# Optimization experiments

Measured on AMD Instinct MI355X. Metric: run time of the kernel, lower is better.

## Reference

```python
import jax, jax.numpy as jnp
import numpy as np

D_MODEL = 512
N_HEADS = 8
D_K = D_MODEL // N_HEADS


def setup_inputs() -> dict:
    key = jax.random.key(0)
    ks = jax.random.split(key, 7)
    s = 1.0 / np.sqrt(D_MODEL)
    return {
        "x": jax.random.normal(ks[0], (2, 4096, D_MODEL), dtype=jnp.float32),
        "W_q": jax.random.normal(ks[1], (D_MODEL, D_MODEL), dtype=jnp.float32) * s,
        "W_k": jax.random.normal(ks[2], (D_MODEL, D_MODEL), dtype=jnp.float32) * s,
        "W_v": jax.random.normal(ks[3], (D_MODEL, D_MODEL), dtype=jnp.float32) * s,
        "b_v": jax.random.normal(ks[4], (D_MODEL,), dtype=jnp.float32) * s,
        "W_o": jax.random.normal(ks[5], (D_MODEL, D_MODEL), dtype=jnp.float32) * s,
        "b_o": jax.random.normal(ks[6], (D_MODEL,), dtype=jnp.float32) * s,
    }


def _split_heads(t):
    # [N, S, d_model] -> [N, H, S, d_k]
    N, S, _ = t.shape
    return t.reshape(N, S, N_HEADS, D_K).transpose(0, 2, 1, 3)


def reference(x, W_q, W_k, W_v, b_v, W_o, b_o):
    N, S, _ = x.shape
    # nn.Linear computes x @ W.T (+ b)
    Q = _split_heads(x @ W_q.T)
    K = _split_heads(x @ W_k.T)
    V = _split_heads(x @ W_v.T + b_v)
    scale = jnp.sqrt(jnp.asarray(D_K, x.dtype))
    scores = jnp.einsum('nhqd,nhkd->nhqk', Q, K) / scale  # [N,H,S,S]
    causal = jnp.tril(jnp.ones((S, S), dtype=bool))
    scores = jnp.where(causal, scores, -jnp.inf)
    attn = jax.nn.softmax(scores, axis=-1)
    out = jnp.einsum('nhqk,nhkd->nhqd', attn, V)  # [N,H,S,d_k]
    out = out.transpose(0, 2, 1, 3).reshape(N, S, D_MODEL)
    return out @ W_o.T + b_o
```

## Files before the change

### kernel.cpp

```cpp
#include <hip/hip_runtime.h>
#include <hip/hip_bf16.h>

#define NB 2
#define SEQ 4096
#define DM 512
#define NH 8
#define DKH 64
#define MTOT (NB*SEQ)

typedef __attribute__((ext_vector_type(4))) float f32x4;
typedef __attribute__((ext_vector_type(16))) float f32x16;
typedef __attribute__((ext_vector_type(8))) short bf16x8;
typedef __attribute__((ext_vector_type(2))) unsigned uint2v;

__device__ inline unsigned short f2bf(float f) {
    union { float f; unsigned int u; } v; v.f = f;
    unsigned int r = v.u + 0x7FFFu + ((v.u >> 16) & 1u);
    return (unsigned short)(r >> 16);
}
__device__ inline float bf2f(unsigned short u) {
    union { unsigned int v; float f; } x; x.v = ((unsigned int)u) << 16; return x.f;
}

#define QSCALE 0.18033688011112042f

__global__ void cast_kernel(const float* __restrict__ x, const float* __restrict__ wq,
                            const float* __restrict__ wk, const float* __restrict__ wv,
                            const float* __restrict__ wo, unsigned short* __restrict__ dst) {
    const int NX = MTOT*DM;
    const int NW = DM*DM;
    int i4 = blockIdx.x * blockDim.x + threadIdx.x;
    long e = (long)i4 * 4;
    if (e >= NX + 4L*NW) return;
    const float* src; long off;
    if (e < NX)           { src = x;  off = e; }
    else if (e < NX+NW)   { src = wq; off = e - NX; }
    else if (e < NX+2*NW) { src = wk; off = e - NX - NW; }
    else if (e < NX+3*NW) { src = wv; off = e - NX - 2*NW; }
    else                  { src = wo; off = e - NX - 3*NW; }
    float4 v = *reinterpret_cast<const float4*>(src + off);
    ushort4 o;
    o.x = f2bf(v.x); o.y = f2bf(v.y); o.z = f2bf(v.z); o.w = f2bf(v.w);
    *reinterpret_cast<ushort4*>(dst + e) = o;
}

template<int MODE>
__global__ __launch_bounds__(256, 2) void gemm_bt(
    const unsigned short* __restrict__ A,
    const unsigned short* __restrict__ B,
    const float* __restrict__ bias,
    unsigned short* __restrict__ Qh, unsigned short* __restrict__ Kh,
    unsigned short* __restrict__ Vt,
    float* __restrict__ Cout)
{
    const int K = 512;
    __shared__ __align__(16) unsigned short As[128*64];
    __shared__ __align__(16) unsigned short Bs[128*64];
    int tid = threadIdx.x;
    int wid = tid >> 6, lane = tid & 63;
    int wr = wid >> 1, wc = wid & 1;
    int brow = blockIdx.x * 128;
    int bcol = blockIdx.y * 128;
    int l15 = lane & 15, l4 = lane >> 4;

    f32x4 acc[4][4] = {};

    for (int kt = 0; kt < K/64; ++kt) {
        __syncthreads();
        #pragma unroll
        for (int i = 0; i < 4; ++i) {
            int rbase = i*32 + wid*8;
            int row = rbase + (lane >> 3);
            int csrc = (lane & 7) ^ (row & 7);
            const unsigned short* asrc = A + (long)(brow+row)*K + kt*64 + csrc*8;
            __builtin_amdgcn_global_load_lds(
                (const __attribute__((address_space(1))) unsigned int*)asrc,
                (__attribute__((address_space(3))) unsigned int*)&As[rbase*64], 16, 0, 0);
            const unsigned short* bsrc = B + (long)(bcol+row)*K + kt*64 + csrc*8;
            __builtin_amdgcn_global_load_lds(
                (const __attribute__((address_space(1))) unsigned int*)bsrc,
                (__attribute__((address_space(3))) unsigned int*)&Bs[rbase*64], 16, 0, 0);
        }
        __syncthreads();
        #pragma unroll
        for (int kk = 0; kk < 2; ++kk) {
            bf16x8 af[4], bfr[4];
            #pragma unroll
            for (int mi = 0; mi < 4; ++mi) {
                int row = wr*64 + mi*16 + l15;
                int colb = (kk*32 + l4*8) * 2;
                af[mi] = *reinterpret_cast<const bf16x8*>(
                    reinterpret_cast<const char*>(As) + row*128 + (colb ^ ((row&7)<<4)));
            }
            #pragma unroll
            for (int ni = 0; ni < 4; ++ni) {
                int row = wc*64 + ni*16 + l15;
                int colb = (kk*32 + l4*8) * 2;
                bfr[ni] = *reinterpret_cast<const bf16x8*>(
                    reinterpret_cast<const char*>(Bs) + row*128 + (colb ^ ((row&7)<<4)));
            }
            #pragma unroll
            for (int mi = 0; mi < 4; ++mi)
                #pragma unroll
                for (int ni = 0; ni < 4; ++ni)
                    acc[mi][ni] = __builtin_amdgcn_mfma_f32_16x16x32_bf16(af[mi], bfr[ni], acc[mi][ni], 0, 0, 0);
        }
    }

    #pragma unroll
    for (int mi = 0; mi < 4; ++mi) {
        #pragma unroll
        for (int ni = 0; ni < 4; ++ni) {
            #pragma unroll
            for (int r = 0; r < 4; ++r) {
                int row = brow + wr*64 + mi*16 + l4*4 + r;
                int col = bcol + wc*64 + ni*16 + l15;
                float v = acc[mi][ni][r];
                if (MODE == 0) {
                    int which = col >> 9;
                    int cw = col & 511;
                    int h = cw >> 6, d = cw & 63;
                    int b = row >> 12, s = row & 4095;
                    int bh = b*NH + h;
                    if (which == 0) {
                        Qh[((long)(bh*SEQ + s))*DKH + d] = f2bf(v * QSCALE);
                    } else if (which == 1) {
                        Kh[((long)(bh*SEQ + s))*DKH + d] = f2bf(v);
                    } else {
                        Vt[((long)(bh*DKH + d))*SEQ + s] = f2bf(v + bias[cw]);
                    }
                } else {
                    Cout[(long)row*DM + col] = v + bias[col];
                }
            }
        }
    }
}

#define PV_STEP_M(SV, VLS, KS, B0, OD0, OD1)  do {                                 \
        unsigned c0, c1, c2, c3;                                                   \
        float t0 = SV[B0+0], t1 = SV[B0+1], t2 = SV[B0+2], t3 = SV[B0+3];          \
        float t4 = SV[B0+4], t5 = SV[B0+5], t6 = SV[B0+6], t7 = SV[B0+7];          \
        asm("v_cvt_pk_bf16_f32 %0, %1, %2" : "=v"(c0) : "v"(t0), "v"(t1));         \
        asm("v_cvt_pk_bf16_f32 %0, %1, %2" : "=v"(c1) : "v"(t2), "v"(t3));         \
        asm("v_cvt_pk_bf16_f32 %0, %1, %2" : "=v"(c2) : "v"(t4), "v"(t5));         \
        asm("v_cvt_pk_bf16_f32 %0, %1, %2" : "=v"(c3) : "v"(t6), "v"(t7));         \
        uint2v sw0 = __builtin_amdgcn_permlane32_swap(c0, c2, false, false);       \
        uint2v sw1 = __builtin_amdgcn_permlane32_swap(c1, c3, false, false);       \
        union { unsigned u[4]; bf16x8 v; } pu;                                     \
        pu.u[0] = sw0[0]; pu.u[1] = sw1[0]; pu.u[2] = sw0[1]; pu.u[3] = sw1[1];    \
        bf16x8 vf0 = *reinterpret_cast<const bf16x8*>(VLS + l31*128      + (((KS)*32 + hi*16) ^ swz)); \
        OD0 = __builtin_amdgcn_mfma_f32_32x32x16_bf16(vf0, pu.v, OD0, 0, 0, 0);    \
        bf16x8 vf1 = *reinterpret_cast<const bf16x8*>(VLS + (32+l31)*128 + (((KS)*32 + hi*16) ^ swz)); \
        OD1 = __builtin_amdgcn_mfma_f32_32x32x16_bf16(vf1, pu.v, OD1, 0, 0, 0);    \
    } while (0)

__global__ __launch_bounds__(256, 4) void attn_split(
    const unsigned short* __restrict__ Qh,
    const unsigned short* __restrict__ Kh,
    const unsigned short* __restrict__ Vt,
    unsigned short* __restrict__ pO0, unsigned short* __restrict__ pO1,
    float* __restrict__ pml)
{
    __shared__ __align__(16) unsigned short Kc[2][64*64];
    __shared__ __align__(16) unsigned short Vc[2][64*64];
    const int tid = threadIdx.x;
    const int wid = tid >> 6, lane = tid & 63;
    const int g = wid & 1, p = wid >> 1;
    const int l31 = lane & 31;
    const int hi  = lane >> 5;

    const int id   = blockIdx.x;
    const int xcd  = id & 7;
    const int rest = id >> 3;
    const int bh   = xcd + ((rest & 1) << 3);
    const int rem  = rest >> 1;
    const int t    = 63 - (rem >> 1);
    const int c    = rem & 1;

    const unsigned short* Qbase = Qh + (long)bh*SEQ*DKH;
    const unsigned short* Kbase = Kh + (long)bh*SEQ*DKH;
    const unsigned short* Vbase = Vt + (long)bh*DKH*SEQ;

    const int q0w = t*64 + g*32;
    const int q   = q0w + l31;
    const int nu  = (t >= c) ? (((t - c) >> 1) + 1) : 0;
    const int swz = (l31 & 7) << 4;

    bf16x8 qf[4];
    #pragma unroll
    for (int kk = 0; kk < 4; ++kk)
        qf[kk] = *reinterpret_cast<const bf16x8*>(Qbase + (long)q*DKH + kk*16 + hi*8);

    auto STAGE = [&](int b, int key0) {
        #pragma unroll
        for (int ii = 0; ii < 2; ++ii) {
            const int rbase = wid*16 + ii*8;
            const int row = rbase + (lane >> 3);
            const int ck = (lane & 7) ^ (row & 7);
            const unsigned short* ksrc = Kbase + (long)(key0 + row)*DKH + ck*8;
            __builtin_amdgcn_global_load_lds(
                (const __attribute__((address_space(1))) unsigned int*)ksrc,
                (__attribute__((address_space(3))) unsigned int*)&Kc[b][rbase*64], 16, 0, 0);
            const unsigned short* vsrc = Vbase + (long)row*SEQ + key0 + ck*8;
            __builtin_amdgcn_global_load_lds(
                (const __attribute__((address_space(1))) unsigned int*)vsrc,
                (__attribute__((address_space(3))) unsigned int*)&Vc[b][rbase*64], 16, 0, 0);
        }
    };

    float m = -1e30f, lsum = 0.f;
    f32x16 od0 = {}, od1 = {};

    if (nu > 0) STAGE(0, c << 6);
    __syncthreads();
    int cur = 0;

    #pragma unroll 1
    for (int s = 0; s < nu; ++s) {
        const int u = c + 2*s;
        if (s + 1 < nu) STAGE(cur ^ 1, (u + 2) << 6);
        const char* kl = reinterpret_cast<const char*>(&Kc[cur][0]) + p*32*128;
        const char* vl = reinterpret_cast<const char*>(&Vc[cur][0]);

        bf16x8 kfr[4];
        #pragma unroll
        for (int kk = 0; kk < 4; ++kk)
            kfr[kk] = *reinterpret_cast<const bf16x8*>(kl + l31*128 + ((kk*32 + hi*16) ^ swz));
        f32x16 sv = {};
        __builtin_amdgcn_s_setprio(1);
        #pragma unroll
        for (int kk = 0; kk < 4; ++kk)
            sv = __builtin_amdgcn_mfma_f32_32x32x16_bf16(kfr[kk], qf[kk], sv, 0, 0, 0);
        __builtin_amdgcn_s_setprio(0);

        if (u == t) {
            const int kbase = (u << 6) + (p << 5);
            #pragma unroll
            for (int r = 0; r < 16; ++r) {
                const int ko = (r&3) + 8*(r>>2) + 4*hi;
                if (kbase + ko > q) sv[r] = -1e30f;
            }
        }

        float m0 = fmaxf(sv[0],  fmaxf(sv[1],  sv[2]));
        float m1 = fmaxf(sv[3],  fmaxf(sv[4],  sv[5]));
        float m2 = fmaxf(sv[6],  fmaxf(sv[7],  sv[8]));
        float m3 = fmaxf(sv[9],  fmaxf(sv[10], sv[11]));
        float m4 = fmaxf(sv[12], fmaxf(sv[13], sv[14]));
        float pmax = fmaxf(fmaxf(m0, fmaxf(m1, m2)), fmaxf(sv[15], fmaxf(m3, m4)));
        {
            uint2v pr = __builtin_amdgcn_permlane32_swap(__float_as_uint(pmax), __float_as_uint(pmax), false, false);
            pmax = fmaxf(__uint_as_float(pr[0]), __uint_as_float(pr[1]));
        }
        if (__any(pmax > m + 6.0f)) {
            const float mn = fmaxf(m, pmax);
            const float alpha = __builtin_amdgcn_exp2f(m - mn);
            m = mn;
            lsum *= alpha;
            #pragma unroll
            for (int r = 0; r < 16; ++r) { od0[r] *= alpha; od1[r] *= alpha; }
        }

        float rs = 0.f;
        #pragma unroll
        for (int r = 0; r < 16; ++r) {
            sv[r] = __builtin_amdgcn_exp2f(sv[r] - m);
            rs += sv[r];
        }
        lsum += rs;

        __builtin_amdgcn_s_setprio(1);
        PV_STEP_M(sv, vl, (2*p),     0, od0, od1);
        PV_STEP_M(sv, vl, (2*p + 1), 8, od0, od1);
        __builtin_amdgcn_s_setprio(0);

        __syncthreads();
        cur ^= 1;
    }

    char*  sod = reinterpret_cast<char*>(&Kc[g][0]);
    float* sml = reinterpret_cast<float*>(&Vc[g][0]);
    const int lswz = (lane & 7) << 4;
    if (p == 1) {
        #pragma unroll
        for (int i = 0; i < 4; ++i) {
            *reinterpret_cast<f32x4*>(sod + lane*128 + ((i*16) ^ lswz)) =
                (f32x4){od0[i*4+0], od0[i*4+1], od0[i*4+2], od0[i*4+3]};
            *reinterpret_cast<f32x4*>(sod + lane*128 + (((i+4)*16) ^ lswz)) =
                (f32x4){od1[i*4+0], od1[i*4+1], od1[i*4+2], od1[i*4+3]};
        }
        sml[lane*2]     = m;
        sml[lane*2 + 1] = lsum;
    }
    __syncthreads();
    if (p == 0) {
        const float pm  = sml[lane*2];
        const float plv = sml[lane*2 + 1];
        const float mn = fmaxf(m, pm);
        const float a0 = __builtin_amdgcn_exp2f(m - mn);
        const float a1 = __builtin_amdgcn_exp2f(pm - mn);
        m = mn;
        lsum = lsum*a0 + plv*a1;
        #pragma unroll
        for (int i = 0; i < 4; ++i) {
            f32x4 t0 = *reinterpret_cast<const f32x4*>(sod + lane*128 + ((i*16) ^ lswz));
            f32x4 t1 = *reinterpret_cast<const f32x4*>(sod + lane*128 + (((i+4)*16) ^ lswz));
            #pragma unroll
            for (int k = 0; k < 4; ++k) {
                od0[i*4+k] = od0[i*4+k]*a0 + t0[k]*a1;
                od1[i*4+k] = od1[i*4+k]*a0 + t1[k]*a1;
            }
        }
        {
            uint2v pr = __builtin_amdgcn_permlane32_swap(__float_as_uint(lsum), __float_as_uint(lsum), false, false);
            lsum = __uint_as_float(pr[0]) + __uint_as_float(pr[1]);
        }
        const int rowg = (bh << 12) + (t << 6) + (g << 5) + l31;
        unsigned short* pO = (c ? pO1 : pO0) + (long)rowg*64;
        #pragma unroll
        for (int rr = 0; rr < 4; ++rr) {
            ushort4 w0, w1;
            w0.x = f2bf(od0[rr*4+0]); w0.y = f2bf(od0[rr*4+1]);
            w0.z = f2bf(od0[rr*4+2]); w0.w = f2bf(od0[rr*4+3]);
            *reinterpret_cast<ushort4*>(pO + rr*8 + hi*4) = w0;
            w1.x = f2bf(od1[rr*4+0]); w1.y = f2bf(od1[rr*4+1]);
            w1.z = f2bf(od1[rr*4+2]); w1.w = f2bf(od1[rr*4+3]);
            *reinterpret_cast<ushort4*>(pO + 32 + rr*8 + hi*4) = w1;
        }
        if (hi == 0) {
            float* base = pml + c*131072;
            base[rowg]         = m;
            base[65536 + rowg] = lsum;
        }
    }
}

__global__ __launch_bounds__(256) void merge_o(
    const unsigned short* __restrict__ pO0, const unsigned short* __restrict__ pO1,
    const float* __restrict__ pml, unsigned short* __restrict__ Obf)
{
    const int tg  = blockIdx.x * 256 + threadIdx.x;
    const int row = tg >> 3;
    const int db  = (tg & 7) * 8;
    const float m0 = pml[row],          l0 = pml[65536 + row];
    const float m1 = pml[131072 + row], l1 = pml[131072 + 65536 + row];
    const float mn = fmaxf(m0, m1);
    const float a0 = __builtin_amdgcn_exp2f(m0 - mn);
    const float a1 = __builtin_amdgcn_exp2f(m1 - mn);
    const float rls = 1.0f / (l0*a0 + l1*a1);
    const float w0 = a0 * rls, w1 = a1 * rls;
    bf16x8 v0 = *reinterpret_cast<const bf16x8*>(pO0 + (long)row*64 + db);
    bf16x8 v1 = *reinterpret_cast<const bf16x8*>(pO1 + (long)row*64 + db);
    const int bh = row >> 12, s = row & 4095;
    const long tok = ((long)(bh >> 3) << 12) + s;
    const int col = ((bh & 7) << 6) + db;
    union { unsigned short u[8]; bf16x8 v; } out;
    #pragma unroll
    for (int k = 0; k < 8; ++k)
        out.u[k] = f2bf(bf2f((unsigned short)v0[k])*w0 + bf2f((unsigned short)v1[k])*w1);
    *reinterpret_cast<bf16x8*>(Obf + tok*DM + col) = out.v;
}

__global__ __launch_bounds__(256, 2) void attn_r9(
    const unsigned short* __restrict__ Qh,
    const unsigned short* __restrict__ Kh,
    const unsigned short* __restrict__ Vt,
    unsigned short* __restrict__ Obf)
{
    __shared__ __align__(16) unsigned short Klds[2][2][64*64];
    __shared__ __align__(16) unsigned short Vlds[2][2][64*64];
    const int tid = threadIdx.x;
    const int wid = tid >> 6, lane = tid & 63;
    const int g = wid & 1, p = wid >> 1;
    const int l31 = lane & 31;
    const int hi  = lane >> 5;
    const int bh  = blockIdx.x;
    const int j   = blockIdx.y;

    const unsigned short* Qbase = Qh + (long)bh*SEQ*DKH;
    const unsigned short* Kbase = Kh + (long)bh*SEQ*DKH;
    const unsigned short* Vbase = Vt + (long)bh*DKH*SEQ;
    const int swz = (l31 & 7) << 4;

    auto STAGE1 = [&](int pb, int b, int key0) {
        #pragma unroll
        for (int ii = 0; ii < 2; ++ii) {
            const int rbase = wid*16 + ii*8;
            const int row = rbase + (lane >> 3);
            const int ck = (lane & 7) ^ (row & 7);
            const unsigned short* ksrc = Kbase + (long)(key0 + row)*DKH + ck*8;
            __builtin_amdgcn_global_load_lds(
                (const __attribute__((address_space(1))) unsigned int*)ksrc,
                (__attribute__((address_space(3))) unsigned int*)&Klds[pb][b][rbase*64], 16, 0, 0);
            const unsigned short* vsrc = Vbase + (long)row*SEQ + key0 + ck*8;
            __builtin_amdgcn_global_load_lds(
                (const __attribute__((address_space(1))) unsigned int*)vsrc,
                (__attribute__((address_space(3))) unsigned int*)&Vlds[pb][b][rbase*64], 16, 0, 0);
        }
    };

    #pragma unroll 1
    for (int half = 0; half < 2; ++half) {
        const int tile = half ? (int)j : 63 - (int)j;
        const int q0w = tile*64 + g*32;
        const int q   = q0w + l31;
        const int nss = (tile >> 1) + 1;

        bf16x8 qf[4];
        #pragma unroll
        for (int kk = 0; kk < 4; ++kk)
            qf[kk] = *reinterpret_cast<const bf16x8*>(Qbase + (long)q*DKH + kk*16 + hi*8);

        float m = -1e30f, lsum = 0.f;
        f32x16 od0 = {}, od1 = {};

        STAGE1(0, 0, 0);
        if (tile >= 1) STAGE1(1, 0, 64);
        __syncthreads();

        #pragma unroll 1
        for (int ss = 0; ss < nss; ++ss) {
            const int nb = (ss + 1) & 1;
            if (2*(ss+1)     <= tile) STAGE1(0, nb, (2*(ss+1))     << 6);
            if (2*(ss+1) + 1 <= tile) STAGE1(1, nb, (2*(ss+1) + 1) << 6);

            const int kb = 2*ss + p;
            if (kb <= tile) {
                const int key0 = kb << 6;
                const char* kl = reinterpret_cast<const char*>(&Klds[p][ss & 1][0]);
                const char* vl = reinterpret_cast<const char*>(&Vlds[p][ss & 1][0]);

                bf16x8 kfr[4][2];
                #pragma unroll
                for (int kk = 0; kk < 4; ++kk) {
                    const int co = (kk*32 + hi*16) ^ swz;
                    kfr[kk][0] = *reinterpret_cast<const bf16x8*>(kl + l31*128      + co);
                    kfr[kk][1] = *reinterpret_cast<const bf16x8*>(kl + (32+l31)*128 + co);
                }
                f32x16 s0 = {}, s1 = {};
                __builtin_amdgcn_s_setprio(1);
                #pragma unroll
                for (int kk = 0; kk < 4; ++kk) {
                    s0 = __builtin_amdgcn_mfma_f32_32x32x16_bf16(kfr[kk][0], qf[kk], s0, 0, 0, 0);
                    s1 = __builtin_amdgcn_mfma_f32_32x32x16_bf16(kfr[kk][1], qf[kk], s1, 0, 0, 0);
                }
                __builtin_amdgcn_s_setprio(0);

                if (kb == tile) {
                    #pragma unroll
                    for (int r = 0; r < 16; ++r) {
                        const int ko = (r&3) + 8*(r>>2) + 4*hi;
                        if (key0 + ko > q)      s0[r] = -1e30f;
                        if (key0 + 32 + ko > q) s1[r] = -1e30f;
                    }
                }

                float pmax = s0[0];
                #pragma unroll
                for (int r = 1; r < 16; ++r) pmax = fmaxf(pmax, s0[r]);
                #pragma unroll
                for (int r = 0; r < 16; ++r) pmax = fmaxf(pmax, s1[r]);
                {
                    uint2v pr = __builtin_amdgcn_permlane32_swap(__float_as_uint(pmax), __float_as_uint(pmax), false, false);
                    pmax = fmaxf(__uint_as_float(pr[0]), __uint_as_float(pr[1]));
                }
                if (__any(pmax > m + 6.0f)) {
                    const float mn = fmaxf(m, pmax);
                    const float alpha = __builtin_amdgcn_exp2f(m - mn);
                    m = mn;
                    lsum *= alpha;
                    #pragma unroll
                    for (int r = 0; r < 16; ++r) { od0[r] *= alpha; od1[r] *= alpha; }
                }

                float rs = 0.f;
                #pragma unroll
                for (int r = 0; r < 16; ++r) { s0[r] = __builtin_amdgcn_exp2f(s0[r] - m); rs += s0[r]; }
                #pragma unroll
                for (int r = 0; r < 16; ++r) { s1[r] = __builtin_amdgcn_exp2f(s1[r] - m); rs += s1[r]; }
                lsum += rs;

                __builtin_amdgcn_s_setprio(1);
                PV_STEP_M(s0, vl, 0, 0, od0, od1);
                PV_STEP_M(s0, vl, 1, 8, od0, od1);
                PV_STEP_M(s1, vl, 2, 0, od0, od1);
                PV_STEP_M(s1, vl, 3, 8, od0, od1);
                __builtin_amdgcn_s_setprio(0);
            }
            __syncthreads();
        }

        char*  sod = reinterpret_cast<char*>(&Klds[g][0][0]);
        float* sml = reinterpret_cast<float*>(&Klds[g][1][0]);
        const int lswz = (lane & 7) << 4;
        if (p == 1) {
            #pragma unroll
            for (int i = 0; i < 4; ++i) {
                *reinterpret_cast<f32x4*>(sod + lane*128 + ((i*16) ^ lswz)) =
                    (f32x4){od0[i*4+0], od0[i*4+1], od0[i*4+2], od0[i*4+3]};
                *reinterpret_cast<f32x4*>(sod + lane*128 + (((i+4)*16) ^ lswz)) =
                    (f32x4){od1[i*4+0], od1[i*4+1], od1[i*4+2], od1[i*4+3]};
            }
            sml[lane*2]     = m;
            sml[lane*2 + 1] = lsum;
        }
        __syncthreads();
        if (p == 0) {
            const float pm  = sml[lane*2];
            const float plv = sml[lane*2 + 1];
            const float mn = fmaxf(m, pm);
            const float a0 = __builtin_amdgcn_exp2f(m - mn);
            const float a1 = __builtin_amdgcn_exp2f(pm - mn);
            lsum = lsum*a0 + plv*a1;
            #pragma unroll
            for (int i = 0; i < 4; ++i) {
                f32x4 t0 = *reinterpret_cast<const f32x4*>(sod + lane*128 + ((i*16) ^ lswz));
                f32x4 t1 = *reinterpret_cast<const f32x4*>(sod + lane*128 + (((i+4)*16) ^ lswz));
                #pragma unroll
                for (int k = 0; k < 4; ++k) {
                    od0[i*4+k] = od0[i*4+k]*a0 + t0[k]*a1;
                    od1[i*4+k] = od1[i*4+k]*a0 + t1[k]*a1;
                }
            }
            {
                uint2v pr = __builtin_amdgcn_permlane32_swap(__float_as_uint(lsum), __float_as_uint(lsum), false, false);
                lsum = __uint_as_float(pr[0]) + __uint_as_float(pr[1]);
            }
            const float rls = 1.0f / lsum;
            const long obase = (long)((bh >> 3)*SEQ + q)*DM + (bh & 7)*DKH;
            #pragma unroll
            for (int rr = 0; rr < 4; ++rr) {
                ushort4 w0, w1;
                w0.x = f2bf(od0[rr*4+0]*rls); w0.y = f2bf(od0[rr*4+1]*rls);
                w0.z = f2bf(od0[rr*4+2]*rls); w0.w = f2bf(od0[rr*4+3]*rls);
                *reinterpret_cast<ushort4*>(Obf + obase + rr*8 + hi*4) = w0;
                w1.x = f2bf(od1[rr*4+0]*rls); w1.y = f2bf(od1[rr*4+1]*rls);
                w1.z = f2bf(od1[rr*4+2]*rls); w1.w = f2bf(od1[rr*4+3]*rls);
                *reinterpret_cast<ushort4*>(Obf + obase + 32 + rr*8 + hi*4) = w1;
            }
        }
        __syncthreads();
    }
}

extern "C" void kernel_launch(void* const* d_in, const int* in_sizes, int n_in,
                              void* d_out, int out_size, void* d_ws, size_t ws_size,
                              hipStream_t stream) {
    const float* x  = (const float*)d_in[0];
    const float* wq = (const float*)d_in[1];
    const float* wk = (const float*)d_in[2];
    const float* wv = (const float*)d_in[3];
    const float* bv = (const float*)d_in[4];
    const float* wo = (const float*)d_in[5];
    const float* bo = (const float*)d_in[6];
    float* out = (float*)d_out;

    unsigned short* ws = (unsigned short*)d_ws;
    unsigned short* Xbf  = ws;
    unsigned short* Wqkv = Xbf  + 4194304;
    unsigned short* Wob  = Wqkv + 786432;
    unsigned short* Qh   = Wob  + 262144;
    unsigned short* Kh   = Qh   + 4194304;
    unsigned short* Vt   = Kh   + 4194304;
    unsigned short* Obf  = Vt   + 4194304;
    unsigned short* pO0  = Obf  + 4194304;
    unsigned short* pO1  = pO0  + 4194304;
    float*          pml  = (float*)(pO1 + 4194304);

    const size_t needed = (size_t)(22020096 + 8388608) * 2 + (size_t)262144 * 4;

    cast_kernel<<<5120, 256, 0, stream>>>(x, wq, wk, wv, wo, Xbf);

    dim3 g1(64, 12);
    gemm_bt<0><<<g1, 256, 0, stream>>>(Xbf, Wqkv, bv, Qh, Kh, Vt, nullptr);

    if (ws_size >= needed) {
        attn_split<<<2048, 256, 0, stream>>>(Qh, Kh, Vt, pO0, pO1, pml);
        merge_o<<<2048, 256, 0, stream>>>(pO0, pO1, pml, Obf);
    } else {
        dim3 g2(16, 32);
        attn_r9<<<g2, 256, 0, stream>>>(Qh, Kh, Vt, Obf);
    }

    dim3 g3(64, 4);
    gemm_bt<1><<<g3, 256, 0, stream>>>(Obf, Wob, bo, nullptr, nullptr, nullptr, out);
}
```

Measured before the change: 112.6 us.

## Fuse split-attention merge into output projection GEMM and double-buffer GEMM tiles

The separate merge_o kernel is folded into a new output-projection GEMM, which combines the two partial attention outputs with their max/sum weights while staging the A tile into LDS. This removes one kernel launch and the write and re-read of the merged O tensor. Both GEMMs also gain double-buffered LDS tiles, so the next K-tile load overlaps the current MFMA work. In exchange, LDS use per block doubles, which may cut occupancy. Each output-column block also redoes the merge arithmetic, repeating it four times across the grid.

```diff
diff --git a/kernel.cpp b/kernel.cpp
--- a/kernel.cpp
+++ b/kernel.cpp
@@ -54,8 +54,8 @@
     float* __restrict__ Cout)
 {
     const int K = 512;
-    __shared__ __align__(16) unsigned short As[128*64];
-    __shared__ __align__(16) unsigned short Bs[128*64];
+    __shared__ __align__(16) unsigned short As[2][128*64];
+    __shared__ __align__(16) unsigned short Bs[2][128*64];
     int tid = threadIdx.x;
     int wid = tid >> 6, lane = tid & 63;
     int wr = wid >> 1, wc = wid & 1;
@@ -63,10 +63,7 @@
     int bcol = blockIdx.y * 128;
     int l15 = lane & 15, l4 = lane >> 4;
 
-    f32x4 acc[4][4] = {};
-
-    for (int kt = 0; kt < K/64; ++kt) {
-        __syncthreads();
+    auto STAGE = [&](int b, int kt) {
         #pragma unroll
         for (int i = 0; i < 4; ++i) {
             int rbase = i*32 + wid*8;
@@ -75,13 +72,21 @@
             const unsigned short* asrc = A + (long)(brow+row)*K + kt*64 + csrc*8;
             __builtin_amdgcn_global_load_lds(
                 (const __attribute__((address_space(1))) unsigned int*)asrc,
-                (__attribute__((address_space(3))) unsigned int*)&As[rbase*64], 16, 0, 0);
+                (__attribute__((address_space(3))) unsigned int*)&As[b][rbase*64], 16, 0, 0);
             const unsigned short* bsrc = B + (long)(bcol+row)*K + kt*64 + csrc*8;
             __builtin_amdgcn_global_load_lds(
                 (const __attribute__((address_space(1))) unsigned int*)bsrc,
-                (__attribute__((address_space(3))) unsigned int*)&Bs[rbase*64], 16, 0, 0);
-        }
-        __syncthreads();
+                (__attribute__((address_space(3))) unsigned int*)&Bs[b][rbase*64], 16, 0, 0);
+        }
+    };
+
+    f32x4 acc[4][4] = {};
+
+    STAGE(0, 0);
+    __syncthreads();
+    int cur = 0;
+    for (int kt = 0; kt < K/64; ++kt) {
+        if (kt + 1 < K/64) STAGE(cur ^ 1, kt + 1);
         #pragma unroll
         for (int kk = 0; kk < 2; ++kk) {
             bf16x8 af[4], bfr[4];
@@ -90,14 +95,14 @@
                 int row = wr*64 + mi*16 + l15;
                 int colb = (kk*32 + l4*8) * 2;
                 af[mi] = *reinterpret_cast<const bf16x8*>(
-                    reinterpret_cast<const char*>(As) + row*128 + (colb ^ ((row&7)<<4)));
+                    reinterpret_cast<const char*>(&As[cur][0]) + row*128 + (colb ^ ((row&7)<<4)));
             }
             #pragma unroll
             for (int ni = 0; ni < 4; ++ni) {
                 int row = wc*64 + ni*16 + l15;
                 int colb = (kk*32 + l4*8) * 2;
                 bfr[ni] = *reinterpret_cast<const bf16x8*>(
-                    reinterpret_cast<const char*>(Bs) + row*128 + (colb ^ ((row&7)<<4)));
+                    reinterpret_cast<const char*>(&Bs[cur][0]) + row*128 + (colb ^ ((row&7)<<4)));
             }
             #pragma unroll
             for (int mi = 0; mi < 4; ++mi)
@@ -105,6 +110,8 @@
                 for (int ni = 0; ni < 4; ++ni)
                     acc[mi][ni] = __builtin_amdgcn_mfma_f32_16x16x32_bf16(af[mi], bfr[ni], acc[mi][ni], 0, 0, 0);
         }
+        __syncthreads();
+        cur ^= 1;
     }
 
     #pragma unroll
@@ -132,6 +139,106 @@
                 } else {
                     Cout[(long)row*DM + col] = v + bias[col];
                 }
+            }
+        }
+    }
+}
+
+__global__ __launch_bounds__(256, 2) void gemm_out(
+    const unsigned short* __restrict__ pO0, const unsigned short* __restrict__ pO1,
+    const float* __restrict__ pml,
+    const unsigned short* __restrict__ B,
+    const float* __restrict__ bias, float* __restrict__ Cout)
+{
+    const int K = 512;
+    __shared__ __align__(16) unsigned short As[2][128*64];
+    __shared__ __align__(16) unsigned short Bs[2][128*64];
+    int tid = threadIdx.x;
+    int wid = tid >> 6, lane = tid & 63;
+    int wr = wid >> 1, wc = wid & 1;
+    int brow = blockIdx.x * 128;
+    int bcol = blockIdx.y * 128;
+    int l15 = lane & 15, l4 = lane >> 4;
+
+    auto STAGE = [&](int b, int kt) {
+        #pragma unroll
+        for (int i = 0; i < 4; ++i) {
+            int rbase = i*32 + wid*8;
+            int row = rbase + (lane >> 3);
+            int csrc = (lane & 7) ^ (row & 7);
+            const unsigned short* bsrc = B + (long)(bcol+row)*K + kt*64 + csrc*8;
+            __builtin_amdgcn_global_load_lds(
+                (const __attribute__((address_space(1))) unsigned int*)bsrc,
+                (__attribute__((address_space(3))) unsigned int*)&Bs[b][rbase*64], 16, 0, 0);
+        }
+        #pragma unroll
+        for (int i = 0; i < 4; ++i) {
+            int rbase = i*32 + wid*8;
+            int row = rbase + (lane >> 3);
+            int tok = brow + row;
+            int ck = (lane & 7) ^ (row & 7);
+            int rowg = (((tok >> 12) << 3) + kt)*4096 + (tok & 4095);
+            bf16x8 v0 = *reinterpret_cast<const bf16x8*>(pO0 + (long)rowg*64 + ck*8);
+            bf16x8 v1 = *reinterpret_cast<const bf16x8*>(pO1 + (long)rowg*64 + ck*8);
+            float m0 = pml[rowg],          l0 = pml[65536 + rowg];
+            float m1 = pml[131072 + rowg], l1 = pml[196608 + rowg];
+            float mn = fmaxf(m0, m1);
+            float a0 = __builtin_amdgcn_exp2f(m0 - mn);
+            float a1 = __builtin_amdgcn_exp2f(m1 - mn);
+            float rls = 1.0f / (l0*a0 + l1*a1);
+            float w0 = a0*rls, w1 = a1*rls;
+            union { unsigned short u[8]; bf16x8 v; } o;
+            #pragma unroll
+            for (int k = 0; k < 8; ++k)
+                o.u[k] = f2bf(bf2f((unsigned short)v0[k])*w0 + bf2f((unsigned short)v1[k])*w1);
+            *reinterpret_cast<bf16x8*>(
+                reinterpret_cast<char*>(&As[b][0]) + row*128 + (lane & 7)*16) = o.v;
+        }
+    };
+
+    f32x4 acc[4][4] = {};
+
+    STAGE(0, 0);
+    __syncthreads();
+    int cur = 0;
+    for (int kt = 0; kt < K/64; ++kt) {
+        if (kt + 1 < K/64) STAGE(cur ^ 1, kt + 1);
+        #pragma unroll
+        for (int kk = 0; kk < 2; ++kk) {
+            bf16x8 af[4], bfr[4];
+            #pragma unroll
+            for (int mi = 0; mi < 4; ++mi) {
+                int row = wr*64 + mi*16 + l15;
+                int colb = (kk*32 + l4*8) * 2;
+                af[mi] = *reinterpret_cast<const bf16x8*>(
+                    reinterpret_cast<const char*>(&As[cur][0]) + row*128 + (colb ^ ((row&7)<<4)));
+            }
+            #pragma unroll
+            for (int ni = 0; ni < 4; ++ni) {
+                int row = wc*64 + ni*16 + l15;
+                int colb = (kk*32 + l4*8) * 2;
+                bfr[ni] = *reinterpret_cast<const bf16x8*>(
+                    reinterpret_cast<const char*>(&Bs[cur][0]) + row*128 + (colb ^ ((row&7)<<4)));
+            }
+            #pragma unroll
+            for (int mi = 0; mi < 4; ++mi)
+                #pragma unroll
+                for (int ni = 0; ni < 4; ++ni)
+                    acc[mi][ni] = __builtin_amdgcn_mfma_f32_16x16x32_bf16(af[mi], bfr[ni], acc[mi][ni], 0, 0, 0);
+        }
+        __syncthreads();
+        cur ^= 1;
+    }
+
+    #pragma unroll
+    for (int mi = 0; mi < 4; ++mi) {
+        #pragma unroll
+        for (int ni = 0; ni < 4; ++ni) {
+            #pragma unroll
+            for (int r = 0; r < 4; ++r) {
+                int row = brow + wr*64 + mi*16 + l4*4 + r;
+                int col = bcol + wc*64 + ni*16 + l15;
+                Cout[(long)row*DM + col] = acc[mi][ni][r] + bias[col];
             }
         }
     }
@@ -575,14 +682,13 @@
     dim3 g1(64, 12);
     gemm_bt<0><<<g1, 256, 0, stream>>>(Xbf, Wqkv, bv, Qh, Kh, Vt, nullptr);
 
+    dim3 g3(64, 4);
     if (ws_size >= needed) {
         attn_split<<<2048, 256, 0, stream>>>(Qh, Kh, Vt, pO0, pO1, pml);
-        merge_o<<<2048, 256, 0, stream>>>(pO0, pO1, pml, Obf);
+        gemm_out<<<g3, 256, 0, stream>>>(pO0, pO1, pml, Wob, bo, out);
     } else {
         dim3 g2(16, 32);
         attn_r9<<<g2, 256, 0, stream>>>(Qh, Kh, Vt, Obf);
-    }
-
-    dim3 g3(64, 4);
-    gemm_bt<1><<<g3, 256, 0, stream>>>(Obf, Wob, bo, nullptr, nullptr, nullptr, out);
-}
+        gemm_bt<1><<<g3, 256, 0, stream>>>(Obf, Wob, bo, nullptr, nullptr, nullptr, out);
+    }
+}
```

Measured after the change: 120.0 us. 6.6% more time.

## Fuse split-KV merge into attention kernel via last-arriver atomic counter

Applied to the files above, without the earlier changes.

Removes the separate merge_o launch. Each attention block now writes its partial output and its m/l statistics with agent-scope atomic stores, then increments a per-(bh,tile) counter. The second block to arrive does the merge and writes Obf. The counters are zeroed inside the cast kernel. This saves one kernel launch and its read of the partials, at the cost of atomic stores and loads, a threadfence, and a serialized merge tail in some blocks.

```diff
diff --git a/kernel.cpp b/kernel.cpp
--- a/kernel.cpp
+++ b/kernel.cpp
@@ -12,6 +12,7 @@
 typedef __attribute__((ext_vector_type(16))) float f32x16;
 typedef __attribute__((ext_vector_type(8))) short bf16x8;
 typedef __attribute__((ext_vector_type(2))) unsigned uint2v;
+typedef unsigned long long ull;
 
 __device__ inline unsigned short f2bf(float f) {
     union { float f; unsigned int u; } v; v.f = f;
@@ -26,10 +27,12 @@
 
 __global__ void cast_kernel(const float* __restrict__ x, const float* __restrict__ wq,
                             const float* __restrict__ wk, const float* __restrict__ wv,
-                            const float* __restrict__ wo, unsigned short* __restrict__ dst) {
+                            const float* __restrict__ wo, unsigned short* __restrict__ dst,
+                            int* __restrict__ ctr) {
     const int NX = MTOT*DM;
     const int NW = DM*DM;
     int i4 = blockIdx.x * blockDim.x + threadIdx.x;
+    if (i4 < 1024) ctr[i4] = 0;
     long e = (long)i4 * 4;
     if (e >= NX + 4L*NW) return;
     const float* src; long off;
@@ -160,10 +163,12 @@
     const unsigned short* __restrict__ Kh,
     const unsigned short* __restrict__ Vt,
     unsigned short* __restrict__ pO0, unsigned short* __restrict__ pO1,
-    float* __restrict__ pml)
+    float* __restrict__ pml, int* __restrict__ ctr,
+    unsigned short* __restrict__ Obf)
 {
     __shared__ __align__(16) unsigned short Kc[2][64*64];
     __shared__ __align__(16) unsigned short Vc[2][64*64];
+    __shared__ int sflag;
     const int tid = threadIdx.x;
     const int wid = tid >> 6, lane = tid & 63;
     const int g = wid & 1, p = wid >> 1;
@@ -317,49 +322,66 @@
             lsum = __uint_as_float(pr[0]) + __uint_as_float(pr[1]);
         }
         const int rowg = (bh << 12) + (t << 6) + (g << 5) + l31;
-        unsigned short* pO = (c ? pO1 : pO0) + (long)rowg*64;
+        ull* pOu = reinterpret_cast<ull*>((c ? pO1 : pO0) + (long)rowg*64);
         #pragma unroll
         for (int rr = 0; rr < 4; ++rr) {
             ushort4 w0, w1;
             w0.x = f2bf(od0[rr*4+0]); w0.y = f2bf(od0[rr*4+1]);
             w0.z = f2bf(od0[rr*4+2]); w0.w = f2bf(od0[rr*4+3]);
-            *reinterpret_cast<ushort4*>(pO + rr*8 + hi*4) = w0;
             w1.x = f2bf(od1[rr*4+0]); w1.y = f2bf(od1[rr*4+1]);
             w1.z = f2bf(od1[rr*4+2]); w1.w = f2bf(od1[rr*4+3]);
-            *reinterpret_cast<ushort4*>(pO + 32 + rr*8 + hi*4) = w1;
+            __hip_atomic_store(&pOu[rr*2 + hi],     *reinterpret_cast<ull*>(&w0),
+                               __ATOMIC_RELAXED, __HIP_MEMORY_SCOPE_AGENT);
+            __hip_atomic_store(&pOu[8 + rr*2 + hi], *reinterpret_cast<ull*>(&w1),
+                               __ATOMIC_RELAXED, __HIP_MEMORY_SCOPE_AGENT);
         }
         if (hi == 0) {
             float* base = pml + c*131072;
-            base[rowg]         = m;
-            base[65536 + rowg] = lsum;
-        }
-    }
-}
-
-__global__ __launch_bounds__(256) void merge_o(
-    const unsigned short* __restrict__ pO0, const unsigned short* __restrict__ pO1,
-    const float* __restrict__ pml, unsigned short* __restrict__ Obf)
-{
-    const int tg  = blockIdx.x * 256 + threadIdx.x;
-    const int row = tg >> 3;
-    const int db  = (tg & 7) * 8;
-    const float m0 = pml[row],          l0 = pml[65536 + row];
-    const float m1 = pml[131072 + row], l1 = pml[131072 + 65536 + row];
-    const float mn = fmaxf(m0, m1);
-    const float a0 = __builtin_amdgcn_exp2f(m0 - mn);
-    const float a1 = __builtin_amdgcn_exp2f(m1 - mn);
-    const float rls = 1.0f / (l0*a0 + l1*a1);
-    const float w0 = a0 * rls, w1 = a1 * rls;
-    bf16x8 v0 = *reinterpret_cast<const bf16x8*>(pO0 + (long)row*64 + db);
-    bf16x8 v1 = *reinterpret_cast<const bf16x8*>(pO1 + (long)row*64 + db);
-    const int bh = row >> 12, s = row & 4095;
-    const long tok = ((long)(bh >> 3) << 12) + s;
-    const int col = ((bh & 7) << 6) + db;
-    union { unsigned short u[8]; bf16x8 v; } out;
-    #pragma unroll
-    for (int k = 0; k < 8; ++k)
-        out.u[k] = f2bf(bf2f((unsigned short)v0[k])*w0 + bf2f((unsigned short)v1[k])*w1);
-    *reinterpret_cast<bf16x8*>(Obf + tok*DM + col) = out.v;
+            __hip_atomic_store(&base[rowg],         m,    __ATOMIC_RELAXED, __HIP_MEMORY_SCOPE_AGENT);
+            __hip_atomic_store(&base[65536 + rowg], lsum, __ATOMIC_RELAXED, __HIP_MEMORY_SCOPE_AGENT);
+        }
+    }
+
+    __syncthreads();
+    if (tid == 0) {
+        __threadfence();
+        int old = __hip_atomic_fetch_add(&ctr[(bh << 6) + t], 1,
+                                         __ATOMIC_ACQ_REL, __HIP_MEMORY_SCOPE_AGENT);
+        sflag = (old == 1);
+    }
+    __syncthreads();
+    if (sflag) {
+        #pragma unroll 1
+        for (int it = tid; it < 512; it += 256) {
+            const int rloc = it >> 3;
+            const int d8   = it & 7;
+            const int rowg = (bh << 12) + (t << 6) + rloc;
+            float m0 = __hip_atomic_load(&pml[rowg],          __ATOMIC_RELAXED, __HIP_MEMORY_SCOPE_AGENT);
+            float l0 = __hip_atomic_load(&pml[65536 + rowg],  __ATOMIC_RELAXED, __HIP_MEMORY_SCOPE_AGENT);
+            float m1 = __hip_atomic_load(&pml[131072 + rowg], __ATOMIC_RELAXED, __HIP_MEMORY_SCOPE_AGENT);
+            float l1 = __hip_atomic_load(&pml[196608 + rowg], __ATOMIC_RELAXED, __HIP_MEMORY_SCOPE_AGENT);
+            const float mn = fmaxf(m0, m1);
+            const float a0 = __builtin_amdgcn_exp2f(m0 - mn);
+            const float a1 = __builtin_amdgcn_exp2f(m1 - mn);
+            const float rls = 1.0f / (l0*a0 + l1*a1);
+            const float w0 = a0*rls, w1 = a1*rls;
+            ull* u0 = reinterpret_cast<ull*>(const_cast<unsigned short*>(pO0) + (long)rowg*64);
+            ull* u1 = reinterpret_cast<ull*>(const_cast<unsigned short*>(pO1) + (long)rowg*64);
+            union { ull u[2]; unsigned short s[8]; } A0, A1;
+            A0.u[0] = __hip_atomic_load(&u0[d8*2],     __ATOMIC_RELAXED, __HIP_MEMORY_SCOPE_AGENT);
+            A0.u[1] = __hip_atomic_load(&u0[d8*2 + 1], __ATOMIC_RELAXED, __HIP_MEMORY_SCOPE_AGENT);
+            A1.u[0] = __hip_atomic_load(&u1[d8*2],     __ATOMIC_RELAXED, __HIP_MEMORY_SCOPE_AGENT);
+            A1.u[1] = __hip_atomic_load(&u1[d8*2 + 1], __ATOMIC_RELAXED, __HIP_MEMORY_SCOPE_AGENT);
+            union { unsigned short s[8]; bf16x8 v; } out;
+            #pragma unroll
+            for (int k = 0; k < 8; ++k)
+                out.s[k] = f2bf(bf2f(A0.s[k])*w0 + bf2f(A1.s[k])*w1);
+            const int s = rowg & 4095;
+            const long tok = ((long)(bh >> 3) << 12) + s;
+            const int col = ((bh & 7) << 6) + d8*8;
+            *reinterpret_cast<bf16x8*>(Obf + tok*DM + col) = out.v;
+        }
+    }
 }
 
 __global__ __launch_bounds__(256, 2) void attn_r9(
@@ -567,22 +589,22 @@
     unsigned short* pO0  = Obf  + 4194304;
     unsigned short* pO1  = pO0  + 4194304;
     float*          pml  = (float*)(pO1 + 4194304);
-
-    const size_t needed = (size_t)(22020096 + 8388608) * 2 + (size_t)262144 * 4;
-
-    cast_kernel<<<5120, 256, 0, stream>>>(x, wq, wk, wv, wo, Xbf);
+    int*            ctr  = (int*)(pml + 262144);
+
+    const size_t needed = 61870080ULL;
+
+    cast_kernel<<<5120, 256, 0, stream>>>(x, wq, wk, wv, wo, Xbf, ctr);
 
     dim3 g1(64, 12);
     gemm_bt<0><<<g1, 256, 0, stream>>>(Xbf, Wqkv, bv, Qh, Kh, Vt, nullptr);
 
+    dim3 g3(64, 4);
     if (ws_size >= needed) {
-        attn_split<<<2048, 256, 0, stream>>>(Qh, Kh, Vt, pO0, pO1, pml);
-        merge_o<<<2048, 256, 0, stream>>>(pO0, pO1, pml, Obf);
+        attn_split<<<2048, 256, 0, stream>>>(Qh, Kh, Vt, pO0, pO1, pml, ctr, Obf);
+        gemm_bt<1><<<g3, 256, 0, stream>>>(Obf, Wob, bo, nullptr, nullptr, nullptr, out);
     } else {
         dim3 g2(16, 32);
         attn_r9<<<g2, 256, 0, stream>>>(Qh, Kh, Vt, Obf);
-    }
-
-    dim3 g3(64, 4);
-    gemm_bt<1><<<g3, 256, 0, stream>>>(Obf, Wob, bo, nullptr, nullptr, nullptr, out);
+        gemm_bt<1><<<g3, 256, 0, stream>>>(Obf, Wob, bo, nullptr, nullptr, nullptr, out);
+    }
 }
```

Result: slower. 205.1 us (+82.2%).
